# Performance work log

Measured on AMD Instinct MI355X. Metric: run time of the kernel, lower is better.

The kernel has to match this reference:

```python
import jax, jax.numpy as jnp
import numpy as np

N, C, B, NPG, M, E = 131072, 128, 64, 2048, 64, 1048576
LN_EPS = 1e-5


def setup_inputs() -> dict:
    key = jax.random.key(0)
    ks = jax.random.split(key, 8)
    h = jax.random.normal(ks[0], (N, C), dtype=jnp.float32)
    edge_index = jax.random.randint(ks[1], (2, E), 0, N, dtype=jnp.int32)
    U = jax.random.normal(ks[2], (B, NPG, M), dtype=jnp.float32)
    W = jax.random.normal(ks[3], (M, C, C), dtype=jnp.float32) * 0.02
    lin_w = jax.random.normal(ks[4], (C, C), dtype=jnp.float32) * (1.0 / np.sqrt(C))
    lin_b = jax.random.normal(ks[5], (C,), dtype=jnp.float32) * 0.01
    ln_g = jnp.ones((C,), dtype=jnp.float32)
    ln_beta = jnp.zeros((C,), dtype=jnp.float32)
    return {"h": h, "U": U, "W": W, "lin_w": lin_w, "lin_b": lin_b,
            "ln_g": ln_g, "ln_beta": ln_beta, "edge_index": edge_index}


def _gfno_block(h, U, W, lin_w, lin_b, ln_g, ln_beta, edge_index):
    n_nodes, c = h.shape
    b, npg, m_avail = U.shape
    m = min(m_avail, W.shape[0])
    Um = U[:, :, :m]                      # [B, n, m]
    Wm = W[:m]                            # [m, C, C]
    # Block-diagonal spectral conv (equal-sized graphs -> batched einsum)
    hb = h.reshape(b, npg, c)             # [B, n, C]
    h_hat = jnp.einsum('bnm,bnc->bmc', Um, hb)        # U^T h per graph
    out_hat = jnp.einsum('bmc,mco->bmo', h_hat, Wm)   # per-mode mixing
    spec = jnp.einsum('bnm,bmo->bno', Um, out_hat).reshape(n_nodes, c)
    # Local scatter-mean aggregation
    src, dst = edge_index[0], edge_index[1]
    agg = jax.ops.segment_sum(h[src], dst, num_segments=n_nodes)   # [N, C]
    deg = jax.ops.segment_sum(jnp.ones((src.shape[0],), h.dtype), dst,
                              num_segments=n_nodes)
    deg = jnp.maximum(deg, 1.0)[:, None]
    local = (agg / deg) @ lin_w.T + lin_b
    # Residual + LayerNorm + GELU (exact, erf-based as torch default)
    x = h + spec + local
    mu = jnp.mean(x, axis=-1, keepdims=True)
    var = jnp.mean(jnp.square(x - mu), axis=-1, keepdims=True)
    xn = (x - mu) * jax.lax.rsqrt(var + LN_EPS) * ln_g + ln_beta
    return jax.nn.gelu(xn, approximate=False)


def reference(h, U, W, lin_w, lin_b, ln_g, ln_beta, edge_index):
    return _gfno_block(h, U, W, lin_w, lin_b, ln_g, ln_beta, edge_index)
```

## Files before the change

### kernel.cpp

```cpp
#include <hip/hip_runtime.h>
#include <math.h>

#define NN   131072
#define CN   128
#define BN   64
#define NPGN 2048
#define MN   64
#define EN   1048576

typedef unsigned short u16;
typedef unsigned int   u32;
typedef __attribute__((ext_vector_type(8))) short short8;
typedef __attribute__((ext_vector_type(4))) float f32x4;

__device__ __forceinline__ float bf2f(u16 u){ return __uint_as_float(((u32)u)<<16); }
__device__ __forceinline__ u16 f2bf(float f){
  u32 x = __float_as_uint(f);
  return (u16)((x + 0x7fffu + ((x>>16)&1u)) >> 16);
}

__global__ void k_count(const int* __restrict__ dst, int* __restrict__ deg){
  int e = blockIdx.x*256 + threadIdx.x;
  atomicAdd(&deg[dst[e]], 1);
}

__global__ void k_scan1(const int* __restrict__ deg, int* __restrict__ rowst, int* __restrict__ bsum){
  __shared__ int s[512];
  const int t = threadIdx.x;
  const int i = blockIdx.x*512 + t;
  int v = deg[i];
  s[t] = v;
  __syncthreads();
  for (int off=1; off<512; off<<=1){
    int a = (t>=off) ? s[t-off] : 0;
    __syncthreads();
    s[t] += a;
    __syncthreads();
  }
  rowst[i] = s[t] - v;
  if (t==511) bsum[blockIdx.x] = s[511];
}

__global__ void k_scan2(const int* __restrict__ bsum, int* __restrict__ bofs){
  __shared__ int s[256];
  const int t = threadIdx.x;
  int v = bsum[t];
  s[t] = v;
  __syncthreads();
  for (int off=1; off<256; off<<=1){
    int a = (t>=off) ? s[t-off] : 0;
    __syncthreads();
    s[t] += a;
    __syncthreads();
  }
  bofs[t] = s[t] - v;
}

__global__ void k_scan3(int* __restrict__ rowst, const int* __restrict__ bofs){
  int i = blockIdx.x*256 + threadIdx.x;
  rowst[i] += bofs[i>>9];
}

__global__ void k_fill(const int* __restrict__ src, const int* __restrict__ dst,
                       const int* __restrict__ rowst, int* __restrict__ cursor,
                       int* __restrict__ csr){
  int e = blockIdx.x*256 + threadIdx.x;
  int d = dst[e];
  int p = atomicAdd(&cursor[d], 1);
  csr[rowst[d] + p] = src[e];
}

__global__ __launch_bounds__(256) void k_prep_all(
    const float* __restrict__ h, u16* __restrict__ h16, u16* __restrict__ ht16,
    const float* __restrict__ U, u16* __restrict__ U16, u16* __restrict__ Ut16,
    const float* __restrict__ lin_w, u16* __restrict__ wsw){
  __shared__ u16 stu[CN*72];
  const int t = threadIdx.x;
  const int bid = blockIdx.x;

  if (bid < 2048){
    const int b = bid >> 5;
    const int n0 = (bid & 31)*64;
    const float* srcb = h + ((size_t)b*NPGN + n0)*CN;
    u16* natb = h16 + ((size_t)b*NPGN + n0)*CN;
    #pragma unroll
    for (int j=0;j<8;++j){
      int fidx = (j*256+t)*4;
      int r = fidx>>7, c = fidx&127;
      float4 v = *(const float4*)(srcb + fidx);
      u16 q0=f2bf(v.x), q1=f2bf(v.y), q2=f2bf(v.z), q3=f2bf(v.w);
      ushort4 nv; nv.x=q0; nv.y=q1; nv.z=q2; nv.w=q3;
      *(ushort4*)(natb + fidx) = nv;
      stu[(c+0)*72 + r] = q0; stu[(c+1)*72 + r] = q1;
      stu[(c+2)*72 + r] = q2; stu[(c+3)*72 + r] = q3;
    }
    __syncthreads();
    #pragma unroll
    for (int j=0;j<4;++j){
      int oidx = (j*256+t)*8;
      int c = oidx>>6, nn = oidx&63;
      uint4 v = *(const uint4*)&stu[c*72 + nn];
      *(uint4*)(ht16 + ((size_t)b*CN + c)*NPGN + n0 + nn) = v;
    }
  } else if (bid < 3072){
    const int ub = bid - 2048;
    const int b = ub >> 4;
    const int n0 = (ub & 15)*128;
    const float* srcb = U + ((size_t)b*NPGN + n0)*MN;
    u16* natb = U16 + ((size_t)b*NPGN + n0)*MN;
    #pragma unroll
    for (int j=0;j<8;++j){
      int fidx = (j*256+t)*4;
      int r = fidx>>6, mm = fidx&63;
      float4 v = *(const float4*)(srcb + fidx);
      u16 q0=f2bf(v.x), q1=f2bf(v.y), q2=f2bf(v.z), q3=f2bf(v.w);
      ushort4 nv; nv.x=q0; nv.y=q1; nv.z=q2; nv.w=q3;
      *(ushort4*)(natb + fidx) = nv;
      stu[(mm+0)*136 + r] = q0; stu[(mm+1)*136 + r] = q1;
      stu[(mm+2)*136 + r] = q2; stu[(mm+3)*136 + r] = q3;
    }
    __syncthreads();
    #pragma unroll
    for (int j=0;j<4;++j){
      int oidx = (j*256+t)*8;
      int mm = oidx>>7, nn = oidx&127;
      uint4 v = *(const uint4*)&stu[mm*136 + nn];
      *(uint4*)(Ut16 + ((size_t)b*MN + mm)*NPGN + n0 + nn) = v;
    }
  } else {
    int tid = (bid - 3072)*256 + t;
    int g = tid >> 6, L = tid & 63;
    int ct = g >> 2, ks = g & 3;
    int o = L & 15, q = L >> 4;
    const float* srcp = lin_w + (ct*16+o)*CN + ks*32 + q*8;
    u16 tmp[8];
    #pragma unroll
    for (int j=0;j<8;++j) tmp[j] = f2bf(srcp[j]);
    *(uint4*)(wsw + (size_t)tid*8) = *(const uint4*)tmp;
  }
}

__global__ void k_prepWT(const float* __restrict__ W, u16* __restrict__ WT16){
  __shared__ u16 st[128*132];
  const int t = threadIdx.x;
  const int m = blockIdx.x;
  const float* Wm = W + (size_t)m*CN*CN;
  #pragma unroll
  for (int it=0; it<16; ++it){
    int flat = (it*256 + t)*4;
    int c = flat >> 7, o = flat & 127;
    float4 v = *(const float4*)(Wm + flat);
    st[(o+0)*132 + c] = f2bf(v.x);
    st[(o+1)*132 + c] = f2bf(v.y);
    st[(o+2)*132 + c] = f2bf(v.z);
    st[(o+3)*132 + c] = f2bf(v.w);
  }
  __syncthreads();
  u16* dstm = WT16 + (size_t)m*CN*CN;
  #pragma unroll
  for (int it=0; it<8; ++it){
    int oidx = (it*256 + t)*8;
    int o = oidx >> 7, c = oidx & 127;
    uint4 v = *(const uint4*)&st[o*132 + c];
    *(uint4*)(dstm + (size_t)o*CN + c) = v;
  }
}

__global__ __launch_bounds__(256) void k_hhat(const u16* __restrict__ Ut16,
                                              const u16* __restrict__ ht16,
                                              float* __restrict__ hp){
  const int t = threadIdx.x;
  const int L = t & 63, w = t >> 6;
  const int b  = blockIdx.x >> 4;
  const int q  = (blockIdx.x >> 1) & 7;
  const int ch = blockIdx.x & 1;
  const int lo = L & 15, qd = (L >> 4) << 3;
  f32x4 acc[4] = {};
  const u16* Arow  = Ut16 + ((size_t)(b*MN + w*16 + lo))*NPGN + q*256 + qd;
  const u16* Bbase = ht16 + ((size_t)(b*CN + ch*64 + lo))*NPGN + q*256 + qd;
  #pragma unroll
  for (int ks=0; ks<8; ++ks){
    short8 af = *(const short8*)(Arow + ks*32);
    #pragma unroll
    for (int ct=0; ct<4; ++ct){
      short8 bf = *(const short8*)(Bbase + (size_t)ct*16*NPGN + ks*32);
      acc[ct] = __builtin_amdgcn_mfma_f32_16x16x32_bf16(af, bf, acc[ct], 0, 0, 0);
    }
  }
  const int rb = w*16 + ((L>>4)<<2);
  float* dstb = hp + ((size_t)q*BN + b)*MN*CN;
  #pragma unroll
  for (int ct=0; ct<4; ++ct)
    #pragma unroll
    for (int r=0; r<4; ++r)
      dstb[(size_t)(rb+r)*CN + ch*64 + ct*16 + lo] = acc[ct][r];
}

__global__ __launch_bounds__(256) void k_ohat(const float* __restrict__ hp,
                                              const u16* __restrict__ WT16,
                                              u16* __restrict__ ohatT){
  __shared__ u16 shHi[16*132];
  __shared__ u16 shLo[16*132];
  const int t = threadIdx.x;
  const int m  = blockIdx.x >> 2;
  const int bq = blockIdx.x & 3;

  {
    const int bl = t >> 4;
    const int c0 = (t & 15) * 8;
    const size_t S = (size_t)BN*MN*CN;
    const float* base = hp + ((size_t)(bq*16 + bl)*MN + m)*CN + c0;
    float a[8] = {0,0,0,0,0,0,0,0};
    #pragma unroll
    for (int q=0; q<8; ++q){
      float4 v0 = *(const float4*)(base + q*S);
      float4 v1 = *(const float4*)(base + q*S + 4);
      a[0]+=v0.x; a[1]+=v0.y; a[2]+=v0.z; a[3]+=v0.w;
      a[4]+=v1.x; a[5]+=v1.y; a[6]+=v1.z; a[7]+=v1.w;
    }
    u16 hi[8], lo[8];
    #pragma unroll
    for (int j=0;j<8;++j){
      hi[j] = f2bf(a[j]);
      lo[j] = f2bf(a[j] - bf2f(hi[j]));
    }
    *(uint4*)&shHi[bl*132 + c0] = *(const uint4*)hi;
    *(uint4*)&shLo[bl*132 + c0] = *(const uint4*)lo;
  }
  __syncthreads();

  const int L = t & 63, w = t >> 6;
  const int lo16 = L & 15, qd = (L >> 4) << 3;
  const u16* WTm = WT16 + (size_t)m*CN*CN;
  f32x4 acc[2] = {};
  #pragma unroll
  for (int ks=0; ks<4; ++ks){
    short8 ah = *(const short8*)&shHi[lo16*132 + ks*32 + qd];
    short8 al = *(const short8*)&shLo[lo16*132 + ks*32 + qd];
    #pragma unroll
    for (int ot=0; ot<2; ++ot){
      short8 bf = *(const short8*)(WTm + (size_t)(w*32 + ot*16 + lo16)*CN + ks*32 + qd);
      acc[ot] = __builtin_amdgcn_mfma_f32_16x16x32_bf16(ah, bf, acc[ot], 0, 0, 0);
      acc[ot] = __builtin_amdgcn_mfma_f32_16x16x32_bf16(al, bf, acc[ot], 0, 0, 0);
    }
  }
  const int rb = (L>>4)<<2;
  #pragma unroll
  for (int ot=0; ot<2; ++ot){
    #pragma unroll
    for (int r=0; r<4; ++r){
      int b = bq*16 + rb + r;
      int o = w*32 + ot*16 + lo16;
      ohatT[((size_t)b*CN + o)*MN + m] = f2bf(acc[ot][r]);
    }
  }
}

__device__ __forceinline__ void unp_fma(float* a, uint4 p, float m){
  a[0]=fmaf(m, bf2f((u16)(p.x&0xffffu)), a[0]); a[1]=fmaf(m, bf2f((u16)(p.x>>16)), a[1]);
  a[2]=fmaf(m, bf2f((u16)(p.y&0xffffu)), a[2]); a[3]=fmaf(m, bf2f((u16)(p.y>>16)), a[3]);
  a[4]=fmaf(m, bf2f((u16)(p.z&0xffffu)), a[4]); a[5]=fmaf(m, bf2f((u16)(p.z>>16)), a[5]);
  a[6]=fmaf(m, bf2f((u16)(p.w&0xffffu)), a[6]); a[7]=fmaf(m, bf2f((u16)(p.w>>16)), a[7]);
}
__device__ __forceinline__ void unp_add(float* a, uint4 p){
  a[0]+=bf2f((u16)(p.x&0xffffu)); a[1]+=bf2f((u16)(p.x>>16));
  a[2]+=bf2f((u16)(p.y&0xffffu)); a[3]+=bf2f((u16)(p.y>>16));
  a[4]+=bf2f((u16)(p.z&0xffffu)); a[5]+=bf2f((u16)(p.z>>16));
  a[6]+=bf2f((u16)(p.w&0xffffu)); a[7]+=bf2f((u16)(p.w>>16));
}

__global__ __launch_bounds__(256,6) void k_localep(
    const u16* __restrict__ h16, const u16* __restrict__ U16,
    const u16* __restrict__ ohatT, const u16* __restrict__ wsw,
    const int* __restrict__ rowst, const int* __restrict__ deg, const int* __restrict__ csr,
    const float* __restrict__ lin_b, const float* __restrict__ ln_g,
    const float* __restrict__ ln_beta, float* __restrict__ out){
  __shared__ u16 sv[32*136];
  __shared__ u16 sx16[32*132];
  const int t = threadIdx.x;
  const int w = t>>6, lane = t&63;
  const size_t n0 = (size_t)blockIdx.x*32;

  {
    const int g   = lane >> 4;
    const int c16 = lane & 15;
    const u16* hcol = h16 + c16*8;
    #pragma unroll
    for (int p=0; p<4; ++p){
      const int iA = p*8 + w;
      const int iB = p*8 + 4 + w;
      const int nA = (int)n0 + iA, nB = (int)n0 + iB;
      const int rsA = rowst[nA], dgA = deg[nA];
      const int rsB = rowst[nB], dgB = deg[nB];
      const int reA = rsA + dgA, reB = rsB + dgB;
      float accA[8] = {0.f,0.f,0.f,0.f,0.f,0.f,0.f,0.f};
      float accB[8] = {0.f,0.f,0.f,0.f,0.f,0.f,0.f,0.f};
      int eA = rsA + g, eB = rsB + g;
      {
        const bool a0 = eA    < reA, a1 = eA+4  < reA, a2 = eA+8  < reA, a3 = eA+12 < reA;
        const bool b0 = eB    < reB, b1 = eB+4  < reB, b2 = eB+8  < reB, b3 = eB+12 < reB;
        int sa0 = csr[a0 ? eA    : 0], sa1 = csr[a1 ? eA+4  : 0];
        int sa2 = csr[a2 ? eA+8  : 0], sa3 = csr[a3 ? eA+12 : 0];
        int sb0 = csr[b0 ? eB    : 0], sb1 = csr[b1 ? eB+4  : 0];
        int sb2 = csr[b2 ? eB+8  : 0], sb3 = csr[b3 ? eB+12 : 0];
        uint4 qa0 = *(const uint4*)(hcol + (size_t)sa0*CN);
        uint4 qa1 = *(const uint4*)(hcol + (size_t)sa1*CN);
        uint4 qa2 = *(const uint4*)(hcol + (size_t)sa2*CN);
        uint4 qa3 = *(const uint4*)(hcol + (size_t)sa3*CN);
        uint4 qb0 = *(const uint4*)(hcol + (size_t)sb0*CN);
        uint4 qb1 = *(const uint4*)(hcol + (size_t)sb1*CN);
        uint4 qb2 = *(const uint4*)(hcol + (size_t)sb2*CN);
        uint4 qb3 = *(const uint4*)(hcol + (size_t)sb3*CN);
        unp_fma(accA, qa0, a0?1.f:0.f); unp_fma(accA, qa1, a1?1.f:0.f);
        unp_fma(accA, qa2, a2?1.f:0.f); unp_fma(accA, qa3, a3?1.f:0.f);
        unp_fma(accB, qb0, b0?1.f:0.f); unp_fma(accB, qb1, b1?1.f:0.f);
        unp_fma(accB, qb2, b2?1.f:0.f); unp_fma(accB, qb3, b3?1.f:0.f);
        eA += 16; eB += 16;
      }
      while (eA < reA || eB < reB){
        const bool a0 = eA < reA, a1 = eA+4 < reA;
        const bool b0 = eB < reB, b1 = eB+4 < reB;
        int sa0 = csr[a0 ? eA   : 0], sa1 = csr[a1 ? eA+4 : 0];
        int sb0 = csr[b0 ? eB   : 0], sb1 = csr[b1 ? eB+4 : 0];
        uint4 qa0 = *(const uint4*)(hcol + (size_t)sa0*CN);
        uint4 qa1 = *(const uint4*)(hcol + (size_t)sa1*CN);
        uint4 qb0 = *(const uint4*)(hcol + (size_t)sb0*CN);
        uint4 qb1 = *(const uint4*)(hcol + (size_t)sb1*CN);
        unp_fma(accA, qa0, a0?1.f:0.f); unp_fma(accA, qa1, a1?1.f:0.f);
        unp_fma(accB, qb0, b0?1.f:0.f); unp_fma(accB, qb1, b1?1.f:0.f);
        eA += 8; eB += 8;
      }
      #pragma unroll
      for (int j=0;j<8;++j){
        accA[j] += __shfl_xor(accA[j],16); accA[j] += __shfl_xor(accA[j],32);
        accB[j] += __shfl_xor(accB[j],16); accB[j] += __shfl_xor(accB[j],32);
      }
      const float invA = 1.0f / fmaxf((float)dgA, 1.0f);
      const float invB = 1.0f / fmaxf((float)dgB, 1.0f);
      if (g==0){
        u16 ta[8], tb[8];
        #pragma unroll
        for (int j=0;j<8;++j){ ta[j]=f2bf(accA[j]*invA); tb[j]=f2bf(accB[j]*invB); }
        *(uint4*)&sv[iA*136 + c16*8] = *(const uint4*)ta;
        *(uint4*)&sv[iB*136 + c16*8] = *(const uint4*)tb;
      }
    }
  }
  __syncthreads();

  const int rt = w&1, cb = w>>1;
  const int lo16 = lane & 15, qd = (lane>>4)<<3;
  f32x4 acc[4] = {};
  #pragma unroll
  for (int ks=0; ks<4; ++ks){
    short8 af = *(const short8*)&sv[(rt*16 + lo16)*136 + ks*32 + qd];
    #pragma unroll
    for (int c4=0; c4<4; ++c4){
      const short8 bf = *(const short8*)(wsw + ((size_t)((cb*4+c4)*4+ks)*64 + lane)*8);
      acc[c4] = __builtin_amdgcn_mfma_f32_16x16x32_bf16(af, bf, acc[c4], 0, 0, 0);
    }
  }
  {
    const int b = (int)(n0 >> 11);
    const u16* Au = U16  + ((size_t)(n0 + rt*16 + lo16))*MN + qd;
    const u16* Bu = ohatT + ((size_t)(b*CN + cb*64 + lo16))*MN + qd;
    #pragma unroll
    for (int ks=0; ks<2; ++ks){
      short8 af = *(const short8*)(Au + ks*32);
      #pragma unroll
      for (int c4=0; c4<4; ++c4){
        short8 bf = *(const short8*)(Bu + (size_t)c4*16*MN + ks*32);
        acc[c4] = __builtin_amdgcn_mfma_f32_16x16x32_bf16(af, bf, acc[c4], 0, 0, 0);
      }
    }
  }
  #pragma unroll
  for (int c4=0; c4<4; ++c4){
    int col = cb*64 + c4*16 + lo16;
    int rb = rt*16 + ((lane>>4)<<2);
    #pragma unroll
    for (int r=0; r<4; ++r) sx16[(rb+r)*132 + col] = f2bf(acc[c4][r]);
  }
  __syncthreads();

  float2 lb    = *(const float2*)(lin_b  + 2*lane);
  float2 lg    = *(const float2*)(ln_g   + 2*lane);
  float2 lbe   = *(const float2*)(ln_beta+ 2*lane);
  for (int r=0; r<8; ++r){
    int i = r*4 + w;
    size_t base = (n0 + i)*CN + 2*lane;
    u32 hA = *(const u32*)(h16 + base);
    u32 lA = *(const u32*)&sx16[i*132 + 2*lane];
    float x0 = bf2f((u16)(hA&0xffffu)) + bf2f((u16)(lA&0xffffu)) + lb.x;
    float x1 = bf2f((u16)(hA>>16))     + bf2f((u16)(lA>>16))     + lb.y;
    float s  = x0 + x1;
    float ss = fmaf(x0,x0, x1*x1);
    #pragma unroll
    for (int d=1; d<64; d<<=1){ s += __shfl_xor(s,d); ss += __shfl_xor(ss,d); }
    float mu  = s*(1.0f/128.0f);
    float var = ss*(1.0f/128.0f) - mu*mu;
    float rstd = rsqrtf(var + 1e-5f);
    float xn0 = (x0-mu)*rstd*lg.x + lbe.x;
    float xn1 = (x1-mu)*rstd*lg.y + lbe.y;
    float2 st;
    st.x = 0.5f*xn0*(1.0f + erff(xn0*0.70710678118654752f));
    st.y = 0.5f*xn1*(1.0f + erff(xn1*0.70710678118654752f));
    *(float2*)(out + base) = st;
  }
}

extern "C" void kernel_launch(void* const* d_in, const int* in_sizes, int n_in,
                              void* d_out, int out_size, void* d_ws, size_t ws_size,
                              hipStream_t stream) {
  const float* h      = (const float*)d_in[0];
  const float* U      = (const float*)d_in[1];
  const float* W      = (const float*)d_in[2];
  const float* lin_w  = (const float*)d_in[3];
  const float* lin_b  = (const float*)d_in[4];
  const float* ln_g   = (const float*)d_in[5];
  const float* ln_b2  = (const float*)d_in[6];
  const int* ei       = (const int*)d_in[7];
  const int* src = ei;
  const int* dst = ei + EN;
  float* out = (float*)d_out;

  char* wp = (char*)d_ws;
  float* hp     = (float*)wp; wp += (size_t)8*BN*MN*CN*sizeof(float);
  u16*   ohatT  = (u16*)wp;   wp += (size_t)BN*CN*MN*sizeof(u16);
  u16*   h16    = (u16*)wp;   wp += (size_t)NN*CN*sizeof(u16);
  u16*   ht16   = (u16*)wp;   wp += (size_t)BN*CN*NPGN*sizeof(u16);
  u16*   U16b   = (u16*)wp;   wp += (size_t)BN*NPGN*MN*sizeof(u16);
  u16*   Ut16   = (u16*)wp;   wp += (size_t)BN*MN*NPGN*sizeof(u16);
  u16*   wsw    = (u16*)wp;   wp += (size_t)CN*CN*sizeof(u16);
  u16*   WT16   = (u16*)wp;   wp += (size_t)MN*CN*CN*sizeof(u16);
  int*   deg    = (int*)wp;   wp += (size_t)NN*sizeof(int);
  int*   rowst  = (int*)wp;   wp += (size_t)NN*sizeof(int);
  int*   cursor = (int*)wp;   wp += (size_t)NN*sizeof(int);
  int*   csr    = (int*)wp;   wp += (size_t)EN*sizeof(int);
  int*   bsum   = (int*)wp;   wp += 512*sizeof(int);
  int*   bofs   = (int*)wp;   wp += 512*sizeof(int);

  hipMemsetAsync(deg,    0, (size_t)NN*sizeof(int), stream);
  hipMemsetAsync(cursor, 0, (size_t)NN*sizeof(int), stream);

  k_count<<<EN/256, 256, 0, stream>>>(dst, deg);
  k_scan1<<<NN/512, 512, 0, stream>>>(deg, rowst, bsum);
  k_scan2<<<1, 256, 0, stream>>>(bsum, bofs);
  k_scan3<<<NN/256, 256, 0, stream>>>(rowst, bofs);
  k_fill<<<EN/256, 256, 0, stream>>>(src, dst, rowst, cursor, csr);

  k_prep_all<<<3080, 256, 0, stream>>>(h, h16, ht16, U, U16b, Ut16, lin_w, wsw);
  k_prepWT<<<MN, 256, 0, stream>>>(W, WT16);

  k_hhat<<<BN*16, 256, 0, stream>>>(Ut16, ht16, hp);
  k_ohat<<<MN*4, 256, 0, stream>>>(hp, WT16, ohatT);

  k_localep<<<NN/32, 256, 0, stream>>>(h16, U16b, ohatT, wsw, rowst, deg, csr,
                                       lin_b, ln_g, ln_b2, out);
}
```

Baseline: 383.5 us.

## Merge scan kernels and prefetch CSR indices with zero-row padding in gather

Result: slower. 455.4 us (+18.7%).

```diff
diff --git a/kernel.cpp b/kernel.cpp
--- a/kernel.cpp
+++ b/kernel.cpp
@@ -41,24 +41,18 @@
   if (t==511) bsum[blockIdx.x] = s[511];
 }
 
-__global__ void k_scan2(const int* __restrict__ bsum, int* __restrict__ bofs){
-  __shared__ int s[256];
-  const int t = threadIdx.x;
-  int v = bsum[t];
-  s[t] = v;
-  __syncthreads();
-  for (int off=1; off<256; off<<=1){
-    int a = (t>=off) ? s[t-off] : 0;
-    __syncthreads();
-    s[t] += a;
-    __syncthreads();
-  }
-  bofs[t] = s[t] - v;
-}
-
-__global__ void k_scan3(int* __restrict__ rowst, const int* __restrict__ bofs){
-  int i = blockIdx.x*256 + threadIdx.x;
-  rowst[i] += bofs[i>>9];
+__global__ void k_scan23(int* __restrict__ rowst, const int* __restrict__ bsum){
+  __shared__ int sred[4];
+  const int t = threadIdx.x;
+  const int gidx = blockIdx.x >> 1;
+  int v = (t < gidx) ? bsum[t] : 0;
+  #pragma unroll
+  for (int d=1; d<64; d<<=1) v += __shfl_xor(v, d);
+  if ((t&63)==0) sred[t>>6] = v;
+  __syncthreads();
+  int tot = sred[0]+sred[1]+sred[2]+sred[3];
+  int i = blockIdx.x*256 + t;
+  rowst[i] += tot;
 }
 
 __global__ void k_fill(const int* __restrict__ src, const int* __restrict__ dst,
@@ -269,7 +263,7 @@
   a[6]+=bf2f((u16)(p.w&0xffffu)); a[7]+=bf2f((u16)(p.w>>16));
 }
 
-__global__ __launch_bounds__(256,6) void k_localep(
+__global__ __launch_bounds__(256,5) void k_localep(
     const u16* __restrict__ h16, const u16* __restrict__ U16,
     const u16* __restrict__ ohatT, const u16* __restrict__ wsw,
     const int* __restrict__ rowst, const int* __restrict__ deg, const int* __restrict__ csr,
@@ -285,58 +279,62 @@
     const int g   = lane >> 4;
     const int c16 = lane & 15;
     const u16* hcol = h16 + c16*8;
-    #pragma unroll
-    for (int p=0; p<4; ++p){
+    int rsA[4], reA[4], rsB[4], reB[4];
+    #pragma unroll
+    for (int p=0;p<4;++p){
+      const int nA = (int)n0 + p*8 + w;
+      rsA[p] = rowst[nA];   reA[p] = rsA[p] + deg[nA];
+      rsB[p] = rowst[nA+4]; reB[p] = rsB[p] + deg[nA+4];
+    }
+    int ia[4][4], ib[4][4];
+    #pragma unroll
+    for (int p=0;p<4;++p){
+      const int eA = rsA[p] + g, eB = rsB[p] + g;
+      #pragma unroll
+      for (int k=0;k<4;++k){ ia[p][k] = csr[eA + 4*k]; ib[p][k] = csr[eB + 4*k]; }
+    }
+    #pragma unroll
+    for (int p=0;p<4;++p){
       const int iA = p*8 + w;
       const int iB = p*8 + 4 + w;
-      const int nA = (int)n0 + iA, nB = (int)n0 + iB;
-      const int rsA = rowst[nA], dgA = deg[nA];
-      const int rsB = rowst[nB], dgB = deg[nB];
-      const int reA = rsA + dgA, reB = rsB + dgB;
+      const int eA = rsA[p] + g, eB = rsB[p] + g;
       float accA[8] = {0.f,0.f,0.f,0.f,0.f,0.f,0.f,0.f};
       float accB[8] = {0.f,0.f,0.f,0.f,0.f,0.f,0.f,0.f};
-      int eA = rsA + g, eB = rsB + g;
-      {
-        const bool a0 = eA    < reA, a1 = eA+4  < reA, a2 = eA+8  < reA, a3 = eA+12 < reA;
-        const bool b0 = eB    < reB, b1 = eB+4  < reB, b2 = eB+8  < reB, b3 = eB+12 < reB;
-        int sa0 = csr[a0 ? eA    : 0], sa1 = csr[a1 ? eA+4  : 0];
-        int sa2 = csr[a2 ? eA+8  : 0], sa3 = csr[a3 ? eA+12 : 0];
-        int sb0 = csr[b0 ? eB    : 0], sb1 = csr[b1 ? eB+4  : 0];
-        int sb2 = csr[b2 ? eB+8  : 0], sb3 = csr[b3 ? eB+12 : 0];
-        uint4 qa0 = *(const uint4*)(hcol + (size_t)sa0*CN);
-        uint4 qa1 = *(const uint4*)(hcol + (size_t)sa1*CN);
-        uint4 qa2 = *(const uint4*)(hcol + (size_t)sa2*CN);
-        uint4 qa3 = *(const uint4*)(hcol + (size_t)sa3*CN);
-        uint4 qb0 = *(const uint4*)(hcol + (size_t)sb0*CN);
-        uint4 qb1 = *(const uint4*)(hcol + (size_t)sb1*CN);
-        uint4 qb2 = *(const uint4*)(hcol + (size_t)sb2*CN);
-        uint4 qb3 = *(const uint4*)(hcol + (size_t)sb3*CN);
-        unp_fma(accA, qa0, a0?1.f:0.f); unp_fma(accA, qa1, a1?1.f:0.f);
-        unp_fma(accA, qa2, a2?1.f:0.f); unp_fma(accA, qa3, a3?1.f:0.f);
-        unp_fma(accB, qb0, b0?1.f:0.f); unp_fma(accB, qb1, b1?1.f:0.f);
-        unp_fma(accB, qb2, b2?1.f:0.f); unp_fma(accB, qb3, b3?1.f:0.f);
-        eA += 16; eB += 16;
+      uint4 qa[4], qb[4];
+      #pragma unroll
+      for (int k=0;k<4;++k){
+        const int sa = (eA + 4*k < reA[p]) ? ia[p][k] : NN;
+        const int sb = (eB + 4*k < reB[p]) ? ib[p][k] : NN;
+        qa[k] = *(const uint4*)(hcol + (size_t)sa*CN);
+        qb[k] = *(const uint4*)(hcol + (size_t)sb*CN);
       }
-      while (eA < reA || eB < reB){
-        const bool a0 = eA < reA, a1 = eA+4 < reA;
-        const bool b0 = eB < reB, b1 = eB+4 < reB;
-        int sa0 = csr[a0 ? eA   : 0], sa1 = csr[a1 ? eA+4 : 0];
-        int sb0 = csr[b0 ? eB   : 0], sb1 = csr[b1 ? eB+4 : 0];
-        uint4 qa0 = *(const uint4*)(hcol + (size_t)sa0*CN);
-        uint4 qa1 = *(const uint4*)(hcol + (size_t)sa1*CN);
-        uint4 qb0 = *(const uint4*)(hcol + (size_t)sb0*CN);
-        uint4 qb1 = *(const uint4*)(hcol + (size_t)sb1*CN);
-        unp_fma(accA, qa0, a0?1.f:0.f); unp_fma(accA, qa1, a1?1.f:0.f);
-        unp_fma(accB, qb0, b0?1.f:0.f); unp_fma(accB, qb1, b1?1.f:0.f);
-        eA += 8; eB += 8;
+      #pragma unroll
+      for (int k=0;k<4;++k){ unp_add(accA, qa[k]); unp_add(accB, qb[k]); }
+      int e2A = eA + 16, e2B = eB + 16;
+      if (__builtin_expect(e2A < reA[p] || e2B < reB[p], 0)){
+        do {
+          const bool a0 = e2A < reA[p], a1 = e2A+4 < reA[p];
+          const bool b0 = e2B < reB[p], b1 = e2B+4 < reB[p];
+          int sa0 = a0 ? csr[a0 ? e2A   : 0] : NN;
+          int sa1 = a1 ? csr[a1 ? e2A+4 : 0] : NN;
+          int sb0 = b0 ? csr[b0 ? e2B   : 0] : NN;
+          int sb1 = b1 ? csr[b1 ? e2B+4 : 0] : NN;
+          uint4 qa0 = *(const uint4*)(hcol + (size_t)sa0*CN);
+          uint4 qa1 = *(const uint4*)(hcol + (size_t)sa1*CN);
+          uint4 qb0 = *(const uint4*)(hcol + (size_t)sb0*CN);
+          uint4 qb1 = *(const uint4*)(hcol + (size_t)sb1*CN);
+          unp_add(accA, qa0); unp_add(accA, qa1);
+          unp_add(accB, qb0); unp_add(accB, qb1);
+          e2A += 8; e2B += 8;
+        } while (e2A < reA[p] || e2B < reB[p]);
       }
       #pragma unroll
       for (int j=0;j<8;++j){
         accA[j] += __shfl_xor(accA[j],16); accA[j] += __shfl_xor(accA[j],32);
         accB[j] += __shfl_xor(accB[j],16); accB[j] += __shfl_xor(accB[j],32);
       }
-      const float invA = 1.0f / fmaxf((float)dgA, 1.0f);
-      const float invB = 1.0f / fmaxf((float)dgB, 1.0f);
+      const float invA = 1.0f / fmaxf((float)(reA[p]-rsA[p]), 1.0f);
+      const float invB = 1.0f / fmaxf((float)(reB[p]-rsB[p]), 1.0f);
       if (g==0){
         u16 ta[8], tb[8];
         #pragma unroll
@@ -427,7 +425,7 @@
   char* wp = (char*)d_ws;
   float* hp     = (float*)wp; wp += (size_t)8*BN*MN*CN*sizeof(float);
   u16*   ohatT  = (u16*)wp;   wp += (size_t)BN*CN*MN*sizeof(u16);
-  u16*   h16    = (u16*)wp;   wp += (size_t)NN*CN*sizeof(u16);
+  u16*   h16    = (u16*)wp;   wp += (size_t)(NN+1)*CN*sizeof(u16);
   u16*   ht16   = (u16*)wp;   wp += (size_t)BN*CN*NPGN*sizeof(u16);
   u16*   U16b   = (u16*)wp;   wp += (size_t)BN*NPGN*MN*sizeof(u16);
   u16*   Ut16   = (u16*)wp;   wp += (size_t)BN*MN*NPGN*sizeof(u16);
@@ -442,11 +440,11 @@
 
   hipMemsetAsync(deg,    0, (size_t)NN*sizeof(int), stream);
   hipMemsetAsync(cursor, 0, (size_t)NN*sizeof(int), stream);
+  hipMemsetAsync(h16 + (size_t)NN*CN, 0, CN*sizeof(u16), stream);
 
   k_count<<<EN/256, 256, 0, stream>>>(dst, deg);
   k_scan1<<<NN/512, 512, 0, stream>>>(deg, rowst, bsum);
-  k_scan2<<<1, 256, 0, stream>>>(bsum, bofs);
-  k_scan3<<<NN/256, 256, 0, stream>>>(rowst, bofs);
+  k_scan23<<<NN/256, 256, 0, stream>>>(rowst, bsum);
   k_fill<<<EN/256, 256, 0, stream>>>(src, dst, rowst, cursor, csr);
 
   k_prep_all<<<3080, 256, 0, stream>>>(h, h16, ht16, U, U16b, Ut16, lin_w, wsw);
```
